# Kernel tuning notes

Hardware: AMD Instinct MI355X
Metric: run time of the kernel (lower is better)

Reference implementation:

```python
import jax, jax.numpy as jnp
import numpy as np

N_NODES = 20000
N_EDGES = 320000
IN_CH = 512
HEADS = 4
OUT_CH = 128
NEG_SLOPE = 0.2  # PyG GATConv default leaky_relu slope


def setup_inputs() -> dict:
    key = jax.random.key(0)
    k1, k2, k3, k4, k5 = jax.random.split(key, 5)
    x = jax.random.normal(k1, (N_NODES, IN_CH), dtype=jnp.float32)
    edge_index = jax.random.randint(k2, (2, N_EDGES), 0, N_NODES, dtype=jnp.int64)
    # Learned parameters (glorot-ish scaling)
    W = jax.random.normal(k3, (IN_CH, HEADS * OUT_CH), dtype=jnp.float32) * np.float32(1.0 / np.sqrt(IN_CH))
    att_src = jax.random.normal(k4, (HEADS, OUT_CH), dtype=jnp.float32) * np.float32(0.1)
    att_dst = jax.random.normal(k5, (HEADS, OUT_CH), dtype=jnp.float32) * np.float32(0.1)
    bias = jnp.zeros((OUT_CH,), dtype=jnp.float32)
    return {"x": x, "W": W, "att_src": att_src, "att_dst": att_dst, "bias": bias, "edge_index": edge_index}


def reference(x, W, att_src, att_dst, bias, edge_index):
    N = x.shape[0]
    H, C = att_src.shape
    # add self-loops (PyG GATConv default add_self_loops=True)
    loop = jnp.arange(N, dtype=edge_index.dtype)
    ei = jnp.concatenate([edge_index, jnp.stack([loop, loop])], axis=1)
    src, dst = ei[0], ei[1]
    # linear projection: [N, H, C]
    xl = (x @ W).reshape(N, H, C)
    # per-node attention halves: [N, H]
    a_s = jnp.einsum('nhc,hc->nh', xl, att_src)
    a_d = jnp.einsum('nhc,hc->nh', xl, att_dst)
    # per-edge logits + segment softmax over incoming edges (grouped by dst)
    alpha = jax.nn.leaky_relu(a_s[src] + a_d[dst], negative_slope=NEG_SLOPE)  # [E, H]
    amax = jax.ops.segment_max(alpha, dst, num_segments=N)  # every node has a self-loop -> no empty segments
    ae = jnp.exp(alpha - amax[dst])
    denom = jax.ops.segment_sum(ae, dst, num_segments=N)
    alpha = ae / (denom[dst] + 1e-16)
    # weighted scatter-add of source features: [N, H, C]
    out = jax.ops.segment_sum(alpha[:, :, None] * xl[src], dst, num_segments=N)
    # concat=False -> mean over heads, then bias [C]
    out = out.mean(axis=1) + bias
    return jax.nn.elu(out)
```

## Files before the change

### kernel.cpp

```cpp
#include <hip/hip_runtime.h>
#include <math.h>

#define N_NODES 20000
#define N_PAD 20096
#define N_EDGES 320000
#define IN_CH 512
#define HEADS 4
#define OUT_CH 128
#define HC 512
#define NEG_SLOPE 0.2f

#define CVX_BLOCKS 5024
#define CVW_BLOCKS 64
#define CNT_BLOCKS 1250

#define GEMM_WGS 628
#define GEMM_XQ 78
#define GEMM_XR 4

typedef __attribute__((ext_vector_type(8))) short short8;
typedef __attribute__((ext_vector_type(4))) float float4v;

__device__ __forceinline__ int detect_is64(const int* __restrict__ ei32) {
    int is64 = 1;
    #pragma unroll
    for (int i = 0; i < 32; i++) is64 &= (ei32[2 * i + 1] == 0);
    return is64;
}

__device__ __forceinline__ int edge_at(const void* ei, int is64, long long idx) {
    return is64 ? (int)((const long long*)ei)[idx] : ((const int*)ei)[idx];
}

__device__ __forceinline__ unsigned short f2bf(float f) {
    union { float f; unsigned u; } v; v.f = f;
    unsigned r = v.u + 0x7fffu + ((v.u >> 16) & 1u);
    return (unsigned short)(r >> 16);
}

__device__ __forceinline__ void bf8_decode(uint4 r, float* f) {
    f[0] = __uint_as_float(r.x << 16); f[1] = __uint_as_float(r.x & 0xffff0000u);
    f[2] = __uint_as_float(r.y << 16); f[3] = __uint_as_float(r.y & 0xffff0000u);
    f[4] = __uint_as_float(r.z << 16); f[5] = __uint_as_float(r.z & 0xffff0000u);
    f[6] = __uint_as_float(r.w << 16); f[7] = __uint_as_float(r.w & 0xffff0000u);
}

__device__ __forceinline__ float leaky(float t) { return t > 0.f ? t : NEG_SLOPE * t; }

__device__ __forceinline__ float sel_head(float4 w, int hd) {
    float lo = (hd & 1) ? w.y : w.x;
    float hi = (hd & 1) ? w.w : w.z;
    return (hd & 2) ? hi : lo;
}

__global__ __launch_bounds__(256) void fusedA_kernel(const float* __restrict__ x,
                                                     const float* __restrict__ W,
                                                     unsigned short* __restrict__ xb,
                                                     unsigned short* __restrict__ Wt,
                                                     const void* __restrict__ ei,
                                                     int* __restrict__ counts,
                                                     int* __restrict__ epos) {
    __shared__ float tile[64][65];
    int b = blockIdx.x;
    if (b < CVX_BLOCKS) {
        size_t i = ((size_t)b * 256 + threadIdx.x) * 8;
        unsigned short o[8];
        if (i < (size_t)N_NODES * IN_CH) {
            float4 f0 = *(const float4*)&x[i];
            float4 f1 = *(const float4*)&x[i + 4];
            o[0] = f2bf(f0.x); o[1] = f2bf(f0.y); o[2] = f2bf(f0.z); o[3] = f2bf(f0.w);
            o[4] = f2bf(f1.x); o[5] = f2bf(f1.y); o[6] = f2bf(f1.z); o[7] = f2bf(f1.w);
        } else {
            for (int k = 0; k < 8; k++) o[k] = 0;
        }
        *(short8*)&xb[i] = *(short8*)o;
    } else if (b < CVX_BLOCKS + CVW_BLOCKS) {
        int idx = b - CVX_BLOCKS;
        int k0 = (idx & 7) * 64, n0 = (idx >> 3) * 64;
        int t = threadIdx.x, r = t >> 6, c = t & 63;
        for (int rr = r; rr < 64; rr += 4)
            tile[rr][c] = W[(size_t)(k0 + rr) * HC + n0 + c];
        __syncthreads();
        for (int rr = r; rr < 64; rr += 4)
            Wt[(size_t)(n0 + rr) * IN_CH + k0 + c] = f2bf(tile[c][rr]);
    } else {
        int is64 = detect_is64((const int*)ei);
        int e = (b - CVX_BLOCKS - CVW_BLOCKS) * 256 + threadIdx.x;
        if (e < N_EDGES) {
            int dst = edge_at(ei, is64, (long long)N_EDGES + e);
            int p = atomicAdd(&counts[dst], 1);
            epos[e] = p;
        }
    }
}

__global__ __launch_bounds__(256, 3) void gemm_kernel(const unsigned short* __restrict__ A,
                                                      const unsigned short* __restrict__ Bt,
                                                      unsigned short* __restrict__ Cb,
                                                      const float* __restrict__ att_s,
                                                      const float* __restrict__ att_d,
                                                      float* __restrict__ a_s,
                                                      float* __restrict__ a_d) {
    __shared__ __align__(16) unsigned short As[2][64 * 32];
    __shared__ __align__(16) unsigned short Bs[2][256 * 32];

    const int bid = blockIdx.x;
    const int xcd = bid & 7, rank = bid >> 3;
    const int w = (xcd < GEMM_XR) ? xcd * (GEMM_XQ + 1) + rank
                                  : GEMM_XR * (GEMM_XQ + 1) + (xcd - GEMM_XR) * GEMM_XQ + rank;
    const int bm = (w >> 1) * 64;
    const int bn = (w & 1) * 256;

    const int t = threadIdx.x;
    const int wv = t >> 6, lane = t & 63;
    const int wm = wv & 1, wn = wv >> 1;
    const int lm = lane & 15, lk = lane >> 4;

    float4v acc[2][8];
    #pragma unroll
    for (int i = 0; i < 2; i++)
        #pragma unroll
        for (int j = 0; j < 8; j++) acc[i][j] = (float4v){0.f, 0.f, 0.f, 0.f};

    const int srow = t >> 2;
    const int sk   = ((t & 3) ^ ((t >> 3) & 3)) * 8;
    const int swr  = (lk ^ ((lm >> 1) & 3)) * 8;

#define GEMM_STAGE(buf, kof)                                                                   \
    {                                                                                          \
        const unsigned short* gA = A + (size_t)(bm + srow) * IN_CH + (kof) + sk;               \
        __builtin_amdgcn_global_load_lds((const __attribute__((address_space(1))) void*)gA,    \
            (__attribute__((address_space(3))) void*)&As[buf][t * 8], 16, 0, 0);               \
        _Pragma("unroll")                                                                      \
        for (int q = 0; q < 4; q++) {                                                          \
            const unsigned short* gB = Bt + (size_t)(bn + q * 64 + srow) * IN_CH + (kof) + sk; \
            __builtin_amdgcn_global_load_lds((const __attribute__((address_space(1))) void*)gB,\
                (__attribute__((address_space(3))) void*)&Bs[buf][q * 2048 + t * 8], 16, 0, 0);\
        }                                                                                      \
    }

    GEMM_STAGE(0, 0);
    #pragma unroll
    for (int kk = 0; kk < 16; ++kk) {
        const int cur = kk & 1;
        if (kk < 15) {
            GEMM_STAGE(cur ^ 1, (kk + 1) * 32);
            asm volatile("s_waitcnt vmcnt(5)" ::: "memory");
        } else {
            asm volatile("s_waitcnt vmcnt(0)" ::: "memory");
        }
        __builtin_amdgcn_s_barrier();
        __builtin_amdgcn_sched_barrier(0);

        short8 af[2], bf[8];
        #pragma unroll
        for (int i = 0; i < 2; i++)
            af[i] = *(const short8*)&As[cur][(wm * 32 + i * 16 + lm) * 32 + swr];
        #pragma unroll
        for (int j = 0; j < 8; j++)
            bf[j] = *(const short8*)&Bs[cur][(wn * 128 + j * 16 + lm) * 32 + swr];
        #pragma unroll
        for (int i = 0; i < 2; i++)
            #pragma unroll
            for (int j = 0; j < 8; j++)
                acc[i][j] = __builtin_amdgcn_mfma_f32_16x16x32_bf16(af[i], bf[j], acc[i][j], 0, 0, 0);

        __builtin_amdgcn_sched_barrier(0);
        __builtin_amdgcn_s_barrier();
    }
#undef GEMM_STAGE

    #pragma unroll
    for (int i = 0; i < 2; i++) {
        #pragma unroll
        for (int r = 0; r < 4; r++) {
            int row = bm + wm * 32 + i * 16 + lk * 4 + r;
            if (row < N_NODES) {
                #pragma unroll
                for (int j = 0; j < 8; j++) {
                    int col = bn + wn * 128 + j * 16 + lm;
                    Cb[(size_t)row * HC + col] = f2bf(acc[i][j][r]);
                }
            }
        }
    }

    const int h = (bn >> 7) + wn;
    float as_w[8], ad_w[8];
    #pragma unroll
    for (int j = 0; j < 8; j++) {
        int col = h * 128 + j * 16 + lm;
        as_w[j] = att_s[col];
        ad_w[j] = att_d[col];
    }
    float ps[2][4], pd[2][4];
    #pragma unroll
    for (int i = 0; i < 2; i++)
        #pragma unroll
        for (int r = 0; r < 4; r++) {
            float s = 0.f, d = 0.f;
            #pragma unroll
            for (int j = 0; j < 8; j++) { s += acc[i][j][r] * as_w[j]; d += acc[i][j][r] * ad_w[j]; }
            ps[i][r] = s; pd[i][r] = d;
        }
    #pragma unroll
    for (int off = 1; off < 16; off <<= 1) {
        #pragma unroll
        for (int i = 0; i < 2; i++)
            #pragma unroll
            for (int r = 0; r < 4; r++) {
                ps[i][r] += __shfl_xor(ps[i][r], off, 64);
                pd[i][r] += __shfl_xor(pd[i][r], off, 64);
            }
    }
    if (lm == 0) {
        #pragma unroll
        for (int i = 0; i < 2; i++)
            #pragma unroll
            for (int r = 0; r < 4; r++) {
                int row = bm + wm * 32 + i * 16 + lk * 4 + r;
                if (row < N_NODES) {
                    a_s[row * 4 + h] = ps[i][r];
                    a_d[row * 4 + h] = pd[i][r];
                }
            }
    }
}

__global__ __launch_bounds__(1024) void scan_kernel(const int* __restrict__ counts,
                                                    int* __restrict__ offsets) {
    const int CHUNK = 20;
    int tid = threadIdx.x;
    int base = tid * CHUNK;
    int c[CHUNK];
    #pragma unroll
    for (int k = 0; k < CHUNK; k++) {
        int i = base + k;
        c[k] = (i < N_NODES) ? counts[i] : 0;
    }
    int pre[CHUNK];
    int sum = 0;
    #pragma unroll
    for (int k = 0; k < CHUNK; k++) { pre[k] = sum; sum += c[k]; }

    int lane = tid & 63, wvv = tid >> 6;
    int s = sum;
    #pragma unroll
    for (int off = 1; off < 64; off <<= 1) {
        int u = __shfl_up(s, off, 64);
        if (lane >= off) s += u;
    }
    __shared__ int wsum[16];
    if (lane == 63) wsum[wvv] = s;
    __syncthreads();
    if (tid < 16) {
        int u = wsum[tid];
        #pragma unroll
        for (int off = 1; off < 16; off <<= 1) {
            int w = __shfl_up(u, off, 64);
            if (tid >= off) u += w;
        }
        wsum[tid] = u;
    }
    __syncthreads();
    int wbase = (wvv == 0) ? 0 : wsum[wvv - 1];
    int excl = wbase + s - sum;
    #pragma unroll
    for (int k = 0; k < CHUNK; k++) {
        int i = base + k;
        if (i < N_NODES) offsets[i] = excl + pre[k];
    }
    if (tid == 1023) offsets[N_NODES] = wbase + s;
}

__global__ __launch_bounds__(256) void scatterw_kernel(const void* __restrict__ ei,
                                                       const int* __restrict__ offsets,
                                                       const int* __restrict__ epos,
                                                       int* __restrict__ sorted_src,
                                                       const float* __restrict__ a_s,
                                                       const float* __restrict__ a_d,
                                                       float* __restrict__ edge_w) {
    int is64 = detect_is64((const int*)ei);
    int e = blockIdx.x * 256 + threadIdx.x;
    if (e < N_EDGES) {
        int dst = edge_at(ei, is64, (long long)N_EDGES + e);
        int src = edge_at(ei, is64, e);
        int pos = offsets[dst] + epos[e];
        sorted_src[pos] = src;
        float4 as4 = *(const float4*)&a_s[src * 4];
        float4 ad4 = *(const float4*)&a_d[dst * 4];
        float4 w;
        w.x = __expf(leaky(as4.x + ad4.x));
        w.y = __expf(leaky(as4.y + ad4.y));
        w.z = __expf(leaky(as4.z + ad4.z));
        w.w = __expf(leaky(as4.w + ad4.w));
        *(float4*)&edge_w[(size_t)pos * 4] = w;
    }
}

__global__ __launch_bounds__(256) void gather_kernel(const unsigned short* __restrict__ xlb,
                                                     const float* __restrict__ a_s,
                                                     const float* __restrict__ a_d,
                                                     const int* __restrict__ offsets,
                                                     const int* __restrict__ sorted_src,
                                                     const float* __restrict__ edge_w,
                                                     const float* __restrict__ bias,
                                                     float* __restrict__ out) {
    __shared__ float cl[2][64][9];
    int wv = threadIdx.x >> 6;
    int nib = wv >> 1;
    int sub = wv & 1;
    int node = blockIdx.x * 2 + nib;
    int lane = threadIdx.x & 63;
    int hd = lane >> 4;
    int beg = offsets[node], end = offsets[node + 1];

    const unsigned short* xrow = xlb + lane * 8;
    float acc[8] = {0, 0, 0, 0, 0, 0, 0, 0};
    float denom = 0.f;

    int c0 = beg + sub * 4;
    int s0 = 0, s1 = 0, s2 = 0, s3 = 0;
    float w0 = 0.f, w1 = 0.f, w2 = 0.f, w3 = 0.f;
    if (c0 < end) {
        int lim = end - 1;
        int i1 = c0 + 1 > lim ? lim : c0 + 1;
        int i2 = c0 + 2 > lim ? lim : c0 + 2;
        int i3 = c0 + 3 > lim ? lim : c0 + 3;
        s0 = sorted_src[c0]; s1 = sorted_src[i1]; s2 = sorted_src[i2]; s3 = sorted_src[i3];
        float4 t0 = *(const float4*)&edge_w[(size_t)c0 * 4];
        float4 t1 = *(const float4*)&edge_w[(size_t)i1 * 4];
        float4 t2 = *(const float4*)&edge_w[(size_t)i2 * 4];
        float4 t3 = *(const float4*)&edge_w[(size_t)i3 * 4];
        w0 = sel_head(t0, hd);
        w1 = (c0 + 1 < end) ? sel_head(t1, hd) : 0.f;
        w2 = (c0 + 2 < end) ? sel_head(t2, hd) : 0.f;
        w3 = (c0 + 3 < end) ? sel_head(t3, hd) : 0.f;
    }

    if (sub == 0) {
        float4 as4 = *(const float4*)&a_s[node * 4];
        float4 ad4 = *(const float4*)&a_d[node * 4];
        float4 ws;
        ws.x = __expf(leaky(as4.x + ad4.x));
        ws.y = __expf(leaky(as4.y + ad4.y));
        ws.z = __expf(leaky(as4.z + ad4.z));
        ws.w = __expf(leaky(as4.w + ad4.w));
        float w = sel_head(ws, hd);
        denom = w;
        uint4 r = *(const uint4*)(xrow + (size_t)node * HC);
        float f[8];
        bf8_decode(r, f);
        #pragma unroll
        for (int k = 0; k < 8; k++) acc[k] = w * f[k];
    }

    for (; c0 < end; c0 += 8) {
        uint4 r0 = *(const uint4*)(xrow + (size_t)s0 * HC);
        uint4 r1 = *(const uint4*)(xrow + (size_t)s1 * HC);
        uint4 r2 = *(const uint4*)(xrow + (size_t)s2 * HC);
        uint4 r3 = *(const uint4*)(xrow + (size_t)s3 * HC);

        int c1 = c0 + 8;
        int n0 = 0, n1 = 0, n2 = 0, n3 = 0;
        float v0 = 0.f, v1 = 0.f, v2 = 0.f, v3 = 0.f;
        if (c1 < end) {
            int lim = end - 1;
            int i1 = c1 + 1 > lim ? lim : c1 + 1;
            int i2 = c1 + 2 > lim ? lim : c1 + 2;
            int i3 = c1 + 3 > lim ? lim : c1 + 3;
            n0 = sorted_src[c1]; n1 = sorted_src[i1]; n2 = sorted_src[i2]; n3 = sorted_src[i3];
            float4 t0 = *(const float4*)&edge_w[(size_t)c1 * 4];
            float4 t1 = *(const float4*)&edge_w[(size_t)i1 * 4];
            float4 t2 = *(const float4*)&edge_w[(size_t)i2 * 4];
            float4 t3 = *(const float4*)&edge_w[(size_t)i3 * 4];
            v0 = sel_head(t0, hd);
            v1 = (c1 + 1 < end) ? sel_head(t1, hd) : 0.f;
            v2 = (c1 + 2 < end) ? sel_head(t2, hd) : 0.f;
            v3 = (c1 + 3 < end) ? sel_head(t3, hd) : 0.f;
        }

        denom += (w0 + w1) + (w2 + w3);
        float f0[8], f1[8], f2[8], f3[8];
        bf8_decode(r0, f0);
        bf8_decode(r1, f1);
        bf8_decode(r2, f2);
        bf8_decode(r3, f3);
        #pragma unroll
        for (int k = 0; k < 8; k++)
            acc[k] += (w0 * f0[k] + w1 * f1[k]) + (w2 * f2[k] + w3 * f3[k]);

        s0 = n0; s1 = n1; s2 = n2; s3 = n3;
        w0 = v0; w1 = v1; w2 = v2; w3 = v3;
    }

    if (sub == 1) {
        #pragma unroll
        for (int k = 0; k < 8; k++) cl[nib][lane][k] = acc[k];
        cl[nib][lane][8] = denom;
    }
    __syncthreads();
    if (sub == 0) {
        #pragma unroll
        for (int k = 0; k < 8; k++) acc[k] += cl[nib][lane][k];
        denom += cl[nib][lane][8];

        float rd = 0.25f / (denom + 1e-16f);
        float v[8];
        #pragma unroll
        for (int k = 0; k < 8; k++) {
            float t = acc[k] * rd;
            t += __shfl_xor(t, 16, 64);
            t += __shfl_xor(t, 32, 64);
            v[k] = t;
        }
        if (hd == 0) {
            float4 b0 = *(const float4*)&bias[lane * 8];
            float4 b1 = *(const float4*)&bias[lane * 8 + 4];
            float o[8];
            o[0] = v[0] + b0.x; o[1] = v[1] + b0.y; o[2] = v[2] + b0.z; o[3] = v[3] + b0.w;
            o[4] = v[4] + b1.x; o[5] = v[5] + b1.y; o[6] = v[6] + b1.z; o[7] = v[7] + b1.w;
            #pragma unroll
            for (int k = 0; k < 8; k++) o[k] = o[k] > 0.f ? o[k] : expm1f(o[k]);
            *(float4*)&out[(size_t)node * OUT_CH + lane * 8]     = make_float4(o[0], o[1], o[2], o[3]);
            *(float4*)&out[(size_t)node * OUT_CH + lane * 8 + 4] = make_float4(o[4], o[5], o[6], o[7]);
        }
    }
}

extern "C" void kernel_launch(void* const* d_in, const int* in_sizes, int n_in,
                              void* d_out, int out_size, void* d_ws, size_t ws_size,
                              hipStream_t stream) {
    const float* x       = (const float*)d_in[0];
    const float* W       = (const float*)d_in[1];
    const float* att_src = (const float*)d_in[2];
    const float* att_dst = (const float*)d_in[3];
    const float* bias    = (const float*)d_in[4];
    const void*  ei      = d_in[5];
    float* out = (float*)d_out;

    char* ws = (char*)d_ws;
    size_t off = 0;
    unsigned short* xlb = (unsigned short*)(ws + off); off += (size_t)N_PAD * HC * sizeof(unsigned short);
    float* a_s     = (float*)(ws + off); off += (size_t)N_NODES * HEADS * sizeof(float);
    float* a_d     = (float*)(ws + off); off += (size_t)N_NODES * HEADS * sizeof(float);
    int* counts    = (int*)(ws + off);   off += (size_t)N_NODES * sizeof(int);
    int* offsets   = (int*)(ws + off);   off += (size_t)(N_NODES + 1) * sizeof(int);
    off = (off + 15) & ~(size_t)15;
    int* epos      = (int*)(ws + off);   off += (size_t)N_EDGES * sizeof(int);
    int* sorted_src = (int*)(ws + off);  off += (size_t)N_EDGES * sizeof(int);
    off = (off + 15) & ~(size_t)15;
    float* edge_w  = (float*)(ws + off); off += (size_t)N_EDGES * HEADS * sizeof(float);
    unsigned short* xb = (unsigned short*)(ws + off); off += (size_t)N_PAD * IN_CH * sizeof(unsigned short);
    unsigned short* Wt = (unsigned short*)(ws + off); off += (size_t)IN_CH * HC * sizeof(unsigned short);

    hipMemsetAsync(counts, 0, N_NODES * sizeof(int), stream);
    fusedA_kernel<<<CVX_BLOCKS + CVW_BLOCKS + CNT_BLOCKS, 256, 0, stream>>>(x, W, xb, Wt, ei, counts, epos);
    gemm_kernel<<<GEMM_WGS, 256, 0, stream>>>(xb, Wt, xlb, att_src, att_dst, a_s, a_d);
    scan_kernel<<<1, 1024, 0, stream>>>(counts, offsets);
    scatterw_kernel<<<(N_EDGES + 255) / 256, 256, 0, stream>>>(ei, offsets, epos, sorted_src, a_s, a_d, edge_w);
    gather_kernel<<<N_NODES / 2, 256, 0, stream>>>(xlb, a_s, a_d, offsets, sorted_src, edge_w, bias, out);
}
```

Before: 208.6 us.

## Split projected features into two channel-half planes and gather per half

The GEMM epilogue now writes the projected bf16 features into two separate planes, each holding 64 channels of every head (256 values per node). The gather kernel assigns one wave per node per channel half, so each gathered row is a contiguous 512-byte segment. This drops the intra-block two-wave split and its shared-memory reduction. The aim is a smaller working set per kernel pass for better cache locality, plus more independent waves. In exchange, source indices and edge weights are read twice, once per half, and each lane issues smaller 8-byte loads.

```diff
diff --git a/kernel.cpp b/kernel.cpp
--- a/kernel.cpp
+++ b/kernel.cpp
@@ -21,6 +21,7 @@
 typedef __attribute__((ext_vector_type(8))) short short8;
 typedef __attribute__((ext_vector_type(4))) float float4v;
 
+
 __device__ __forceinline__ int detect_is64(const int* __restrict__ ei32) {
     int is64 = 1;
     #pragma unroll
@@ -43,6 +44,11 @@
     f[2] = __uint_as_float(r.y << 16); f[3] = __uint_as_float(r.y & 0xffff0000u);
     f[4] = __uint_as_float(r.z << 16); f[5] = __uint_as_float(r.z & 0xffff0000u);
     f[6] = __uint_as_float(r.w << 16); f[7] = __uint_as_float(r.w & 0xffff0000u);
+}
+
+__device__ __forceinline__ void bf4_decode(uint2 r, float* f) {
+    f[0] = __uint_as_float(r.x << 16); f[1] = __uint_as_float(r.x & 0xffff0000u);
+    f[2] = __uint_as_float(r.y << 16); f[3] = __uint_as_float(r.y & 0xffff0000u);
 }
 
 __device__ __forceinline__ float leaky(float t) { return t > 0.f ? t : NEG_SLOPE * t; }
@@ -170,6 +176,7 @@
     }
 #undef GEMM_STAGE
 
+    const int h = (bn >> 7) + wn;
     #pragma unroll
     for (int i = 0; i < 2; i++) {
         #pragma unroll
@@ -178,14 +185,14 @@
             if (row < N_NODES) {
                 #pragma unroll
                 for (int j = 0; j < 8; j++) {
-                    int col = bn + wn * 128 + j * 16 + lm;
-                    Cb[(size_t)row * HC + col] = f2bf(acc[i][j][r]);
+                    int g = j >> 2;
+                    int inhead = (j & 3) * 16 + lm;
+                    Cb[((size_t)g * N_PAD + row) * 256 + h * 64 + inhead] = f2bf(acc[i][j][r]);
                 }
             }
         }
     }
 
-    const int h = (bn >> 7) + wn;
     float as_w[8], ad_w[8];
     #pragma unroll
     for (int j = 0; j < 8; j++) {
@@ -306,20 +313,36 @@
                                                      const float* __restrict__ edge_w,
                                                      const float* __restrict__ bias,
                                                      float* __restrict__ out) {
-    __shared__ float cl[2][64][9];
+    int b = blockIdx.x;
+    int g = b & 1;
     int wv = threadIdx.x >> 6;
-    int nib = wv >> 1;
-    int sub = wv & 1;
-    int node = blockIdx.x * 2 + nib;
+    int node = (b >> 1) * 4 + wv;
     int lane = threadIdx.x & 63;
     int hd = lane >> 4;
     int beg = offsets[node], end = offsets[node + 1];
 
-    const unsigned short* xrow = xlb + lane * 8;
-    float acc[8] = {0, 0, 0, 0, 0, 0, 0, 0};
-    float denom = 0.f;
-
-    int c0 = beg + sub * 4;
+    const unsigned short* xg = xlb + (size_t)g * N_PAD * 256 + lane * 4;
+    float acc[4] = {0, 0, 0, 0};
+    float denom;
+
+    {
+        float4 as4 = *(const float4*)&a_s[node * 4];
+        float4 ad4 = *(const float4*)&a_d[node * 4];
+        float4 ws;
+        ws.x = __expf(leaky(as4.x + ad4.x));
+        ws.y = __expf(leaky(as4.y + ad4.y));
+        ws.z = __expf(leaky(as4.z + ad4.z));
+        ws.w = __expf(leaky(as4.w + ad4.w));
+        float w = sel_head(ws, hd);
+        denom = w;
+        uint2 r = *(const uint2*)(xg + (size_t)node * 256);
+        float f[4];
+        bf4_decode(r, f);
+        #pragma unroll
+        for (int k = 0; k < 4; k++) acc[k] = w * f[k];
+    }
+
+    int c0 = beg;
     int s0 = 0, s1 = 0, s2 = 0, s3 = 0;
     float w0 = 0.f, w1 = 0.f, w2 = 0.f, w3 = 0.f;
     if (c0 < end) {
@@ -338,30 +361,13 @@
         w3 = (c0 + 3 < end) ? sel_head(t3, hd) : 0.f;
     }
 
-    if (sub == 0) {
-        float4 as4 = *(const float4*)&a_s[node * 4];
-        float4 ad4 = *(const float4*)&a_d[node * 4];
-        float4 ws;
-        ws.x = __expf(leaky(as4.x + ad4.x));
-        ws.y = __expf(leaky(as4.y + ad4.y));
-        ws.z = __expf(leaky(as4.z + ad4.z));
-        ws.w = __expf(leaky(as4.w + ad4.w));
-        float w = sel_head(ws, hd);
-        denom = w;
-        uint4 r = *(const uint4*)(xrow + (size_t)node * HC);
-        float f[8];
-        bf8_decode(r, f);
-        #pragma unroll
-        for (int k = 0; k < 8; k++) acc[k] = w * f[k];
-    }
-
-    for (; c0 < end; c0 += 8) {
-        uint4 r0 = *(const uint4*)(xrow + (size_t)s0 * HC);
-        uint4 r1 = *(const uint4*)(xrow + (size_t)s1 * HC);
-        uint4 r2 = *(const uint4*)(xrow + (size_t)s2 * HC);
-        uint4 r3 = *(const uint4*)(xrow + (size_t)s3 * HC);
-
-        int c1 = c0 + 8;
+    for (; c0 < end; c0 += 4) {
+        uint2 r0 = *(const uint2*)(xg + (size_t)s0 * 256);
+        uint2 r1 = *(const uint2*)(xg + (size_t)s1 * 256);
+        uint2 r2 = *(const uint2*)(xg + (size_t)s2 * 256);
+        uint2 r3 = *(const uint2*)(xg + (size_t)s3 * 256);
+
+        int c1 = c0 + 4;
         int n0 = 0, n1 = 0, n2 = 0, n3 = 0;
         float v0 = 0.f, v1 = 0.f, v2 = 0.f, v3 = 0.f;
         if (c1 < end) {
@@ -381,50 +387,37 @@
         }
 
         denom += (w0 + w1) + (w2 + w3);
-        float f0[8], f1[8], f2[8], f3[8];
-        bf8_decode(r0, f0);
-        bf8_decode(r1, f1);
-        bf8_decode(r2, f2);
-        bf8_decode(r3, f3);
-        #pragma unroll
-        for (int k = 0; k < 8; k++)
+        float f0[4], f1[4], f2[4], f3[4];
+        bf4_decode(r0, f0);
+        bf4_decode(r1, f1);
+        bf4_decode(r2, f2);
+        bf4_decode(r3, f3);
+        #pragma unroll
+        for (int k = 0; k < 4; k++)
             acc[k] += (w0 * f0[k] + w1 * f1[k]) + (w2 * f2[k] + w3 * f3[k]);
 
         s0 = n0; s1 = n1; s2 = n2; s3 = n3;
         w0 = v0; w1 = v1; w2 = v2; w3 = v3;
     }
 
-    if (sub == 1) {
-        #pragma unroll
-        for (int k = 0; k < 8; k++) cl[nib][lane][k] = acc[k];
-        cl[nib][lane][8] = denom;
-    }
-    __syncthreads();
-    if (sub == 0) {
-        #pragma unroll
-        for (int k = 0; k < 8; k++) acc[k] += cl[nib][lane][k];
-        denom += cl[nib][lane][8];
-
-        float rd = 0.25f / (denom + 1e-16f);
-        float v[8];
-        #pragma unroll
-        for (int k = 0; k < 8; k++) {
-            float t = acc[k] * rd;
-            t += __shfl_xor(t, 16, 64);
-            t += __shfl_xor(t, 32, 64);
-            v[k] = t;
-        }
-        if (hd == 0) {
-            float4 b0 = *(const float4*)&bias[lane * 8];
-            float4 b1 = *(const float4*)&bias[lane * 8 + 4];
-            float o[8];
-            o[0] = v[0] + b0.x; o[1] = v[1] + b0.y; o[2] = v[2] + b0.z; o[3] = v[3] + b0.w;
-            o[4] = v[4] + b1.x; o[5] = v[5] + b1.y; o[6] = v[6] + b1.z; o[7] = v[7] + b1.w;
-            #pragma unroll
-            for (int k = 0; k < 8; k++) o[k] = o[k] > 0.f ? o[k] : expm1f(o[k]);
-            *(float4*)&out[(size_t)node * OUT_CH + lane * 8]     = make_float4(o[0], o[1], o[2], o[3]);
-            *(float4*)&out[(size_t)node * OUT_CH + lane * 8 + 4] = make_float4(o[4], o[5], o[6], o[7]);
-        }
+    float rd = 0.25f / (denom + 1e-16f);
+    float v[4];
+    #pragma unroll
+    for (int k = 0; k < 4; k++) {
+        float t = acc[k] * rd;
+        t += __shfl_xor(t, 16, 64);
+        t += __shfl_xor(t, 32, 64);
+        v[k] = t;
+    }
+    if (hd == 0) {
+        int cb = g * 64 + lane * 4;
+        float o[4];
+        #pragma unroll
+        for (int k = 0; k < 4; k++) {
+            float t = v[k] + bias[cb + k];
+            o[k] = t > 0.f ? t : expm1f(t);
+        }
+        *(float4*)&out[(size_t)node * OUT_CH + cb] = make_float4(o[0], o[1], o[2], o[3]);
     }
 }
 
@@ -441,7 +434,7 @@
 
     char* ws = (char*)d_ws;
     size_t off = 0;
-    unsigned short* xlb = (unsigned short*)(ws + off); off += (size_t)N_PAD * HC * sizeof(unsigned short);
+    unsigned short* xlb = (unsigned short*)(ws + off); off += (size_t)2 * N_PAD * 256 * sizeof(unsigned short);
     float* a_s     = (float*)(ws + off); off += (size_t)N_NODES * HEADS * sizeof(float);
     float* a_d     = (float*)(ws + off); off += (size_t)N_NODES * HEADS * sizeof(float);
     int* counts    = (int*)(ws + off);   off += (size_t)N_NODES * sizeof(int);
@@ -459,5 +452,5 @@
     gemm_kernel<<<GEMM_WGS, 256, 0, stream>>>(xb, Wt, xlb, att_src, att_dst, a_s, a_d);
     scan_kernel<<<1, 1024, 0, stream>>>(counts, offsets);
     scatterw_kernel<<<(N_EDGES + 255) / 256, 256, 0, stream>>>(ei, offsets, epos, sorted_src, a_s, a_d, edge_w);
-    gather_kernel<<<N_NODES / 2, 256, 0, stream>>>(xlb, a_s, a_d, offsets, sorted_src, edge_w, bias, out);
-}
+    gather_kernel<<<(N_NODES / 4) * 2, 256, 0, stream>>>(xlb, a_s, a_d, offsets, sorted_src, edge_w, bias, out);
+}
```

New measurement: 221.3 us. 6.1% more time.
